# Kernel tuning notes

Hardware: AMD Instinct MI355X
Metric: run time of the kernel (lower is better)

The kernel has to match this reference:

```python
import jax, jax.numpy as jnp
import numpy as np

N_QUBITS = 10
N_LAYERS = 2
QSVT_DEGREE = 3
DT_RANK = 5  # n_qubits // 2
PI = np.float32(np.pi)

# ---- batched statevector simulation helpers (wire 0 = most significant, as in pennylane default.qubit) ----

def _apply_1q(s, wire, U):
    # s: (batch,) + (2,)*n complex; U: (batch,2,2) or (2,2)
    s = jnp.moveaxis(s, 1 + wire, 1)
    shp = s.shape
    s2 = s.reshape(shp[0], 2, -1)
    if U.ndim == 3:
        out = jnp.einsum('bij,bjr->bir', U, s2)
    else:
        out = jnp.einsum('ij,bjr->bir', U, s2)
    return jnp.moveaxis(out.reshape(shp), 1, 1 + wire)

def _ry(t):
    c = jnp.cos(t / 2).astype(jnp.complex64)
    s = jnp.sin(t / 2).astype(jnp.complex64)
    return jnp.stack([jnp.stack([c, -s], -1), jnp.stack([s, c], -1)], -2)

def _rz(t):
    e = jnp.exp(-0.5j * jnp.asarray(t).astype(jnp.complex64))
    z = jnp.zeros_like(e)
    return jnp.stack([jnp.stack([e, z], -1), jnp.stack([z, jnp.conj(e)], -1)], -2)

def _rx(t):
    c = jnp.cos(t / 2).astype(jnp.complex64)
    s = (-1j) * jnp.sin(t / 2).astype(jnp.complex64)
    return jnp.stack([jnp.stack([c, s], -1), jnp.stack([s, c], -1)], -2)

def _cnot(s, control, target):
    f = jnp.flip(s, axis=1 + target)
    s0 = jax.lax.index_in_dim(s, 0, axis=1 + control, keepdims=True)
    f1 = jax.lax.index_in_dim(f, 1, axis=1 + control, keepdims=True)
    return jnp.concatenate([s0, f1], axis=1 + control)

def _circuit(h, x, dt, cp, pc):
    """Batched selective QSVT circuit; h,x,dt: (B,n). Returns <Z_i> per wire, (B,n) float32."""
    n = N_QUBITS
    b = h.shape[0]
    s = jnp.zeros((b, 2 ** n), jnp.complex64).at[:, 0].set(1.0).reshape((b,) + (2,) * n)
    # 1. state encoding
    for i in range(n):
        s = _apply_1q(s, i, _ry(h[:, i]))
    # 2. delta-modulated QSVT block
    for d in range(QSVT_DEGREE + 1):
        for i in range(n):
            s = _apply_1q(s, i, _rz(pc[d] * dt[:, i] * PI))
        for i in range(n - 1):
            s = _cnot(s, i, i + 1)
        s = _cnot(s, n - 1, 0)
    # 3. variational block
    k = 0
    for _ in range(N_LAYERS):
        for i in range(n):
            s = _apply_1q(s, i, _rx(cp[k]))
            s = _apply_1q(s, i, _ry(cp[k + 1]))
            s = _apply_1q(s, i, _rz(cp[k + 2]))
            k += 3
        for i in range(n - 1):
            s = _cnot(s, i, i + 1)
    # 4. delta-modulated input encoding
    for i in range(n):
        s = _apply_1q(s, i, _ry(x[:, i] * dt[:, i]))
    # 5. <Z_i> measurements
    p = s.real ** 2 + s.imag ** 2
    zs = [(jax.lax.index_in_dim(p, 0, 1 + i, False) - jax.lax.index_in_dim(p, 1, 1 + i, False)).reshape(b, -1).sum(-1) for i in range(n)]
    return jnp.stack(zs, -1).astype(jnp.float32)

def setup_inputs() -> dict:
    key = jax.random.key(0)
    ks = jax.random.split(key, 6)
    B, S, n, r = 128, 512, N_QUBITS, DT_RANK
    angles = jax.random.uniform(ks[0], (B, S, n), jnp.float32) * PI  # angle encoding in [0, pi]
    W_x = jax.random.normal(ks[1], (r + 2 * n, n), jnp.float32) * 0.3  # x_proj weight (no bias)
    W_dt = jax.random.normal(ks[2], (n, r), jnp.float32) * 0.3  # dt_proj weight
    rng = np.random.default_rng(0)
    dt0 = np.exp(rng.random(n) * (np.log(0.1) - np.log(0.001)) + np.log(0.001))
    b_dt = jnp.asarray(dt0 + np.log(-np.expm1(-dt0)), jnp.float32)  # inverse-softplus init
    poly_coeffs = jax.random.normal(ks[3], (QSVT_DEGREE + 1,), jnp.float32) * 0.1
    circuit_params = jax.random.normal(ks[4], (n * N_LAYERS * 3,), jnp.float32) * 0.1
    D = jnp.ones((n,), jnp.float32)
    return {"angles": angles, "W_x": W_x, "W_dt": W_dt, "b_dt": b_dt,
            "poly_coeffs": poly_coeffs, "circuit_params": circuit_params, "D": D}

def reference(angles, W_x, W_dt, b_dt, poly_coeffs, circuit_params, D):
    # selective projections
    x_dbc = jnp.einsum('bsn,kn->bsk', angles, W_x)
    dt_raw = x_dbc[..., :DT_RANK]
    # B slice (x_dbc[..., DT_RANK:DT_RANK+n]) is computed but unused in the original forward
    C = x_dbc[..., DT_RANK + N_QUBITS:]
    dt = jax.nn.softplus(jnp.einsum('bsr,nr->bsn', dt_raw, W_dt) + b_dt)
    dt_angles = jnp.tanh(dt) * PI
    # quantum recurrence uses detached tensors in the original (torch .detach())
    x_sg = jax.lax.stop_gradient(angles)
    dt_sg = jax.lax.stop_gradient(dt_angles)
    cp = jax.lax.stop_gradient(circuit_params)
    pc = jax.lax.stop_gradient(poly_coeffs)

    def step(h, xs):
        x_t, d_t = xs
        h2 = _circuit(h, x_t, d_t, cp, pc)
        return h2, h2

    h0 = jnp.zeros((angles.shape[0], N_QUBITS), jnp.float32)
    _, hs = jax.lax.scan(step, h0, (jnp.swapaxes(x_sg, 0, 1), jnp.swapaxes(dt_sg, 0, 1)))
    hs = jnp.swapaxes(hs, 0, 1)  # (B,S,n)
    return C * hs + D * angles
```

## Files before the change

### kernel.cpp

```cpp
#include <hip/hip_runtime.h>
#include <math.h>


#define PIF 3.14159265358979323846f

constexpr int NQ = 10, SEQ = 512, NB = 128, NTHR = 256, RECF = 36;

struct CTbl { int mz[4][NQ]; };
constexpr CTbl build_tbl() {
  CTbl t{};
  unsigned mrow[NQ];
  for (int b = 0; b < NQ; ++b) mrow[b] = 1u << b;
  for (int d = 0; d < 4; ++d) {
    for (int i = 0; i < NQ; ++i) t.mz[d][i] = (int)mrow[9 - i];
    for (int i = 0; i < NQ - 1; ++i) { int bc = 9 - i, bt = 8 - i; mrow[bt] ^= mrow[bc]; }
    mrow[9] ^= mrow[0];
  }
  return t;
}
constexpr CTbl CT = build_tbl();

struct PermCols { int c4[10]; int cL[10]; };
constexpr PermCols build_perms() {
  PermCols P{};
  for (int b = 0; b < 10; ++b) {
    int x = 1 << b;
    for (int d = 0; d < 4; ++d) {
      for (int i = 0; i < 9; ++i) { int bc = 9 - i, bt = 8 - i; if ((x >> bc) & 1) x ^= (1 << bt); }
      if (x & 1) x ^= (1 << 9);
    }
    P.c4[b] = x;
    int y = 1 << b;
    for (int i = 0; i < 9; ++i) { int bc = 9 - i, bt = 8 - i; if ((y >> bc) & 1) y ^= (1 << bt); }
    P.cL[b] = y;
  }
  return P;
}
constexpr PermCols PC = build_perms();

constexpr int lanePart(int x) { return ((x >> 0) & 1) | (((x >> 5) & 1) << 1) |
                                       (((x >> 1) & 1) << 2) | (((x >> 7) & 1) << 3) |
                                       (((x >> 3) & 1) << 4) | (((x >> 9) & 1) << 5); }
constexpr int regPart2(int x)  { return ((x >> 2) & 1) | (((x >> 6) & 1) << 1); }
constexpr int wavePart(int x)  { return ((x >> 4) & 1) | (((x >> 8) & 1) << 1); }

typedef __attribute__((ext_vector_type(2))) float v2;

template<int C>
__device__ __forceinline__ int dpp1(int x) {
  return __builtin_amdgcn_update_dpp(x, x, C, 0xF, 0xF, false);
}
template<int VL>
__device__ __forceinline__ int lxi(int x) {
  if constexpr (VL == 1)  return dpp1<0xB1>(x);
  else if constexpr (VL == 2)  return dpp1<0x4E>(x);
  else if constexpr (VL == 3)  return dpp1<0x1B>(x);
  else if constexpr (VL <= 7) {
    constexpr int q = (VL & 3) ^ 3;
    int y = x;
    if constexpr (q == 1) y = dpp1<0xB1>(y);
    else if constexpr (q == 2) y = dpp1<0x4E>(y);
    else if constexpr (q == 3) y = dpp1<0x1B>(y);
    return dpp1<0x141>(y);
  } else if constexpr (VL >= 12) {
    constexpr int q = (VL & 3) ^ 3;
    int y = x;
    if constexpr (q == 1) y = dpp1<0xB1>(y);
    else if constexpr (q == 2) y = dpp1<0x4E>(y);
    else if constexpr (q == 3) y = dpp1<0x1B>(y);
    return dpp1<0x140>(y);
  } else {
    constexpr int a = VL & 3;
    int y = x;
    if constexpr (a == 1) y = dpp1<0xB1>(y);
    else if constexpr (a == 2) y = dpp1<0x4E>(y);
    else if constexpr (a == 3) y = dpp1<0x1B>(y);
    y = dpp1<0x141>(y);
    return dpp1<0x140>(y);
  }
}
template<int VL>
__device__ __forceinline__ float lx(float x) {
  if constexpr (VL == 0) return x;
  else if constexpr (VL & 32) {
    int addr = (((int)threadIdx.x & 63) ^ VL) << 2;
    return __int_as_float(__builtin_amdgcn_ds_bpermute(addr, __float_as_int(x)));
  } else if constexpr (VL & 16) {
    return __int_as_float(__builtin_amdgcn_ds_swizzle(__float_as_int(x), (VL << 10) | 0x1F));
  } else {
    return __int_as_float(lxi<VL>(__float_as_int(x)));
  }
}
__device__ __forceinline__ float rdl(float x, int l) {
  return __int_as_float(__builtin_amdgcn_readlane(__float_as_int(x), l));
}

__device__ __forceinline__ void apply4(v2* amp, const v2* p, bool par, float4 U0, float4 U1) {
  v2 u00 = {U0.x, U0.y}, u01 = {U0.z, U0.w}, u10 = {U1.x, U1.y}, u11 = {U1.z, U1.w};
  v2 A = par ? u11 : u00, B = par ? u10 : u01;
  v2 An = {-A.y, A.y}, Bn = {-B.y, B.y};
#pragma unroll
  for (int r = 0; r < 4; ++r) {
    v2 o = amp[r], q = p[r];
    v2 res = A.x * o;
    res += An * __builtin_shufflevector(o, o, 1, 0);
    res += B.x * q;
    res += Bn * __builtin_shufflevector(q, q, 1, 0);
    amp[r] = res;
  }
}

template<int VL>
__device__ __forceinline__ void gate_lane(v2* amp, float4 U0, float4 U1, int lane) {
  v2 p[4];
#pragma unroll
  for (int r = 0; r < 4; ++r) { p[r].x = lx<VL>(amp[r].x); p[r].y = lx<VL>(amp[r].y); }
  apply4(amp, p, (lane & VL) != 0, U0, U1);
}

template<int VR>
__device__ __forceinline__ void gate_reg(v2* amp, float4 U0, float4 U1) {
  v2 p[4];
#pragma unroll
  for (int r = 0; r < 4; ++r) p[r] = amp[r ^ VR];
  v2 u00 = {U0.x, U0.y}, u01 = {U0.z, U0.w}, u10 = {U1.x, U1.y}, u11 = {U1.z, U1.w};
#pragma unroll
  for (int r = 0; r < 4; ++r) {
    const bool par = (r & VR) != 0;
    v2 A = par ? u11 : u00, B = par ? u10 : u01;
    v2 An = {-A.y, A.y}, Bn = {-B.y, B.y};
    v2 o = amp[r], q = p[r];
    v2 res = A.x * o;
    res += An * __builtin_shufflevector(o, o, 1, 0);
    res += B.x * q;
    res += Bn * __builtin_shufflevector(q, q, 1, 0);
    amp[r] = res;
  }
}

__device__ __forceinline__ void gate_wave(v2* amp, float4 U0, float4 U1,
                                          v2* exb, int wbase, int pbase, bool par) {
#pragma unroll
  for (int r = 0; r < 4; ++r) exb[r * 256 + wbase] = amp[r];
  __syncthreads();
  v2 p[4];
#pragma unroll
  for (int r = 0; r < 4; ++r) p[r] = exb[r * 256 + pbase];
  apply4(amp, p, par, U0, U1);
}

__device__ __forceinline__ void permute(v2* amp, v2* buf, int dbase, int o1, int o2, int oidx) {
  buf[dbase]           = amp[0];
  buf[dbase ^ o1]      = amp[1];
  buf[dbase ^ o2]      = amp[2];
  buf[dbase ^ o1 ^ o2] = amp[3];
  __syncthreads();
  amp[0] = buf[oidx];
  amp[1] = buf[oidx | 4];
  amp[2] = buf[oidx | 64];
  amp[3] = buf[oidx | 68];
}

template<int VL>
__device__ __forceinline__ float xdot_lane(const v2* amp) {
  v2 acc = {0.f, 0.f};
#pragma unroll
  for (int r = 0; r < 4; ++r) {
    v2 p; p.x = lx<VL>(amp[r].x); p.y = lx<VL>(amp[r].y);
    acc += amp[r] * p;
  }
  return acc.x + acc.y;
}
template<int VR>
__device__ __forceinline__ float xdot_reg(const v2* amp) {
  v2 acc = {0.f, 0.f};
#pragma unroll
  for (int r = 0; r < 4; ++r) acc += amp[r] * amp[r ^ VR];
  return acc.x + acc.y;
}

__global__ __launch_bounds__(NTHR, 1) void qmamba_main(
    const float* __restrict__ angles, const float* __restrict__ Wx,
    const float* __restrict__ Wdt, const float* __restrict__ bdt,
    const float* __restrict__ pc, const float* __restrict__ cp,
    float* __restrict__ out)
{
  __shared__ float  tblL[SEQ][RECF];
  __shared__ float4 uuL[40];
  __shared__ v2     ex0[1024];
  __shared__ v2     ex1[1024];
  __shared__ float  zb[4][16];

  const int tid  = threadIdx.x;
  const int lane = tid & 63;
  const int wave = tid >> 6;
  const int b    = blockIdx.x;

  if (tid < 20) {
    int k = tid * 3;
    float al = 0.5f * cp[k], be = 0.5f * cp[k + 1], ga = 0.5f * cp[k + 2];
    float ca = __cosf(al), sa = __sinf(al);
    float cb = __cosf(be), sb = __sinf(be);
    float cg = __cosf(ga), sg = __sinf(ga);
    float2 M00 = make_float2(cb * ca,  sb * sa);
    float2 M01 = make_float2(-sb * ca, -cb * sa);
    float2 M10 = make_float2(sb * ca,  -cb * sa);
    float2 M11 = make_float2(cb * ca,  -sb * sa);
    float2 e0 = make_float2(cg, -sg), e1 = make_float2(cg, sg);
    auto cm = [](float2 a, float2 c) {
      return make_float2(a.x * c.x - a.y * c.y, a.x * c.y + a.y * c.x);
    };
    float2 u00 = cm(M00, e0), u01 = cm(M01, e0), u10 = cm(M10, e1), u11 = cm(M11, e1);
    uuL[2 * tid]     = make_float4(u00.x, u00.y, u01.x, u01.y);
    uuL[2 * tid + 1] = make_float4(u10.x, u10.y, u11.x, u11.y);
  }

#pragma unroll 1
  for (int k = 0; k < 2; ++k) {
    const int t = k * NTHR + tid;
    const float* ar = angles + (size_t)(b * SEQ + t) * NQ;
    float a[NQ];
#pragma unroll
    for (int n = 0; n < NQ; ++n) a[n] = ar[n];
    float dtr[5];
#pragma unroll
    for (int r = 0; r < 5; ++r) {
      float acc = 0.f;
#pragma unroll
      for (int n = 0; n < NQ; ++n) acc += a[n] * Wx[r * NQ + n];
      dtr[r] = acc;
    }
    float* rec = &tblL[t][0];
#pragma unroll
    for (int w = 0; w < NQ; ++w) {
      float lin = bdt[w];
#pragma unroll
      for (int r = 0; r < 5; ++r) lin += dtr[r] * Wdt[w * 5 + r];
      float sp = lin > 0.f ? lin + log1pf(__expf(-lin)) : log1pf(__expf(lin));
      float th = tanhf(sp) * PIF;
      float fa = a[w] * th;
      rec[w]      = th;
      rec[12 + w] = __cosf(fa);
      rec[24 + w] = __sinf(fa);
    }
  }
  __syncthreads();

  float pch[4];
#pragma unroll
  for (int d = 0; d < 4; ++d) pch[d] = 0.5f * pc[d] * PIF;

  unsigned PW0 = 0, PW1 = 0;
#pragma unroll
  for (int k = 0; k < 40; ++k) {
    const int m  = CT.mz[k / 10][k % 10];
    const int lm = lanePart(m), wm = wavePart(m);
    unsigned flip = ((unsigned)((__popc(lane & lm) ^ __popc(wave & wm)) & 1)) ^ 1u;
    if (k < 32) PW0 |= flip << k; else PW1 |= flip << (k - 32);
  }

  int d4 = 0, dL = 0;
  if (lane & 1)  { d4 ^= PC.c4[0]; dL ^= PC.cL[0]; }
  if (lane & 2)  { d4 ^= PC.c4[5]; dL ^= PC.cL[5]; }
  if (lane & 4)  { d4 ^= PC.c4[1]; dL ^= PC.cL[1]; }
  if (lane & 8)  { d4 ^= PC.c4[7]; dL ^= PC.cL[7]; }
  if (lane & 16) { d4 ^= PC.c4[3]; dL ^= PC.cL[3]; }
  if (lane & 32) { d4 ^= PC.c4[9]; dL ^= PC.cL[9]; }
  if (wave & 1)  { d4 ^= PC.c4[4]; dL ^= PC.cL[4]; }
  if (wave & 2)  { d4 ^= PC.c4[8]; dL ^= PC.cL[8]; }

  const int oidx = (lane & 1) | (((lane >> 1) & 1) << 5) | (((lane >> 2) & 1) << 1)
                 | (((lane >> 3) & 1) << 7) | (((lane >> 4) & 1) << 3) | (((lane >> 5) & 1) << 9)
                 | ((wave & 1) << 4) | (((wave >> 1) & 1) << 8);

  const int wbase = wave * 64 + lane;
  const int pb1   = (wave ^ 1) * 64 + lane;
  const int pb2   = (wave ^ 2) * 64 + lane;

  float hcw[NQ], hsw[NQ];
#pragma unroll
  for (int w = 0; w < NQ; ++w) { hcw[w] = 1.f; hsw[w] = 0.f; }

  v2 amp[4];

#pragma unroll 1
  for (int t = 0; t < SEQ; ++t) {
    float tha[12];
    {
      const float4* rq = (const float4*)&tblL[t][0];
#pragma unroll
      for (int j = 0; j < 3; ++j) ((float4*)tha)[j] = rq[j];
    }

    float F;
    F  = (lane & 1)  ? hsw[9] : hcw[9];
    F *= (lane & 2)  ? hsw[4] : hcw[4];
    F *= (lane & 4)  ? hsw[8] : hcw[8];
    F *= (lane & 8)  ? hsw[2] : hcw[2];
    F *= (lane & 16) ? hsw[6] : hcw[6];
    F *= (lane & 32) ? hsw[0] : hcw[0];
    F *= (wave & 1)  ? hsw[5] : hcw[5];
    F *= (wave & 2)  ? hsw[1] : hcw[1];
    const float G0 = F * hcw[7] * hcw[3];
    const float G1 = F * hsw[7] * hcw[3];
    const float G2 = F * hcw[7] * hsw[3];
    const float G3 = F * hsw[7] * hsw[3];

    float S[4] = {0.f, 0.f, 0.f, 0.f};
#pragma unroll
    for (int k = 0; k < 40; ++k) {
      const int m  = CT.mz[k / 10][k % 10];
      const int gr = regPart2(m);
      float v = pch[k / 10] * tha[k % 10];
      unsigned fl = ((k < 32 ? (PW0 >> k) : (PW1 >> (k - 32))) & 1u) << 31;
      S[gr] += __int_as_float(__float_as_int(v) ^ fl);
    }
    {
      float a0 = S[0], a1 = S[1], a2 = S[2], a3 = S[3];
      float b0 = a0 + a1, b1 = a0 - a1, b2 = a2 + a3, b3 = a2 - a3;
      S[0] = b0 + b2; S[2] = b0 - b2; S[1] = b1 + b3; S[3] = b1 - b3;
    }
    {
      float sn, cs;
      __sincosf(S[0], &sn, &cs); amp[0].x = G0 * cs; amp[0].y = G0 * sn;
      __sincosf(S[1], &sn, &cs); amp[1].x = G1 * cs; amp[1].y = G1 * sn;
      __sincosf(S[2], &sn, &cs); amp[2].x = G2 * cs; amp[2].y = G2 * sn;
      __sincosf(S[3], &sn, &cs); amp[3].x = G3 * cs; amp[3].y = G3 * sn;
    }

    permute(amp, ex0, d4, PC.c4[2], PC.c4[6], oidx);

    gate_lane<32>(amp, uuL[0],  uuL[1],  lane);
    gate_wave    (amp, uuL[2],  uuL[3],  ex1, wbase, pb2, (wave & 2) != 0);
    gate_lane<8> (amp, uuL[4],  uuL[5],  lane);
    gate_reg<2>  (amp, uuL[6],  uuL[7]);
    gate_lane<2> (amp, uuL[8],  uuL[9],  lane);
    gate_wave    (amp, uuL[10], uuL[11], ex0, wbase, pb1, (wave & 1) != 0);
    gate_lane<16>(amp, uuL[12], uuL[13], lane);
    gate_reg<1>  (amp, uuL[14], uuL[15]);
    gate_lane<4> (amp, uuL[16], uuL[17], lane);
    gate_lane<1> (amp, uuL[18], uuL[19], lane);

    permute(amp, ex1, dL, PC.cL[2], PC.cL[6], oidx);

    gate_lane<32>(amp, uuL[20], uuL[21], lane);
    gate_wave    (amp, uuL[22], uuL[23], ex0, wbase, pb2, (wave & 2) != 0);
    gate_lane<8> (amp, uuL[24], uuL[25], lane);
    gate_reg<2>  (amp, uuL[26], uuL[27]);
    gate_lane<2> (amp, uuL[28], uuL[29], lane);
    gate_wave    (amp, uuL[30], uuL[31], ex1, wbase, pb1, (wave & 1) != 0);
    gate_lane<16>(amp, uuL[32], uuL[33], lane);
    gate_reg<1>  (amp, uuL[34], uuL[35]);
    gate_lane<4> (amp, uuL[36], uuL[37], lane);
    gate_lane<1> (amp, uuL[38], uuL[39], lane);

    permute(amp, ex0, dL, PC.cL[2], PC.cL[6], oidx);

    float cfv[12], sfv[12];
    {
      const float4* rq = (const float4*)&tblL[t][0];
#pragma unroll
      for (int j = 0; j < 3; ++j) { ((float4*)cfv)[j] = rq[3 + j]; ((float4*)sfv)[j] = rq[6 + j]; }
    }

    float T[4];
#pragma unroll
    for (int r = 0; r < 4; ++r) T[r] = amp[r].x * amp[r].x + amp[r].y * amp[r].y;
    {
      float a0 = T[0], a1 = T[1], a2 = T[2], a3 = T[3];
      float b0 = a0 + a1, b1 = a0 - a1, b2 = a2 + a3, b3 = a2 - a3;
      T[0] = b0 + b2; T[2] = b0 - b2; T[1] = b1 + b3; T[3] = b1 - b3;
    }

    v2 pw1[4], pw5[4];
    {
#pragma unroll
      for (int r = 0; r < 4; ++r) ex1[r * 256 + wbase] = amp[r];
      __syncthreads();
#pragma unroll
      for (int r = 0; r < 4; ++r) pw1[r] = ex1[r * 256 + pb2];
#pragma unroll
      for (int r = 0; r < 4; ++r) pw5[r] = ex1[r * 256 + pb1];
    }

    float zv[NQ];
    { float zp = (lane & 32) ? -T[0] : T[0]; zv[0] = cfv[0] * zp - sfv[0] * xdot_lane<32>(amp); }
    { float zp = (wave & 2)  ? -T[0] : T[0];
      v2 acc = {0.f, 0.f};
#pragma unroll
      for (int r = 0; r < 4; ++r) acc += amp[r] * pw1[r];
      zv[1] = cfv[1] * zp - sfv[1] * (acc.x + acc.y); }
    { float zp = (lane & 8)  ? -T[0] : T[0]; zv[2] = cfv[2] * zp - sfv[2] * xdot_lane<8>(amp); }
    { zv[3] = cfv[3] * T[2] - sfv[3] * xdot_reg<2>(amp); }
    { float zp = (lane & 2)  ? -T[0] : T[0]; zv[4] = cfv[4] * zp - sfv[4] * xdot_lane<2>(amp); }
    { float zp = (wave & 1)  ? -T[0] : T[0];
      v2 acc = {0.f, 0.f};
#pragma unroll
      for (int r = 0; r < 4; ++r) acc += amp[r] * pw5[r];
      zv[5] = cfv[5] * zp - sfv[5] * (acc.x + acc.y); }
    { float zp = (lane & 16) ? -T[0] : T[0]; zv[6] = cfv[6] * zp - sfv[6] * xdot_lane<16>(amp); }
    { zv[7] = cfv[7] * T[1] - sfv[7] * xdot_reg<1>(amp); }
    { float zp = (lane & 4)  ? -T[0] : T[0]; zv[8] = cfv[8] * zp - sfv[8] * xdot_lane<4>(amp); }
    { float zp = (lane & 1)  ? -T[0] : T[0]; zv[9] = cfv[9] * zp - sfv[9] * xdot_lane<1>(amp); }

#pragma unroll
    for (int w = 0; w < NQ; ++w) {
      zv[w] += lx<1>(zv[w]);
      zv[w] += lx<2>(zv[w]);
      zv[w] += lx<4>(zv[w]);
    }
    const int l7 = lane & 7;
    float c01 = (l7 & 1) ? zv[1] : zv[0];
    float c23 = (l7 & 1) ? zv[3] : zv[2];
    float c45 = (l7 & 1) ? zv[5] : zv[4];
    float c67 = (l7 & 1) ? zv[7] : zv[6];
    float c03 = (l7 & 2) ? c23 : c01;
    float c47 = (l7 & 2) ? c67 : c45;
    float pk  = (l7 & 4) ? c47 : c03;
    pk += lx<8>(pk);  pk += lx<16>(pk);  pk += lx<32>(pk);
    float z8 = zv[8]; z8 += lx<8>(z8); z8 += lx<16>(z8); z8 += lx<32>(z8);
    float z9 = zv[9]; z9 += lx<8>(z9); z9 += lx<16>(z9); z9 += lx<32>(z9);
    float zsel = pk;
    zsel = (lane == 8) ? z8 : zsel;
    zsel = (lane == 9) ? z9 : zsel;

    if (lane < NQ) zb[wave][lane] = zsel;
    __syncthreads();
    float z = 0.f;
    if (lane < NQ) {
      z = zb[0][lane] + zb[1][lane] + zb[2][lane] + zb[3][lane];
      if (wave == 0) out[(size_t)(b * SEQ + t) * NQ + lane] = z;
    }
    float sn_h, cs_h;
    __sincosf(0.5f * z, &sn_h, &cs_h);
#pragma unroll
    for (int w = 0; w < NQ; ++w) { hcw[w] = rdl(cs_h, w); hsw[w] = rdl(sn_h, w); }
  }
}

__global__ __launch_bounds__(256) void qmamba_post(
    const float* __restrict__ angles, const float* __restrict__ Wx,
    const float* __restrict__ Dg, float* __restrict__ out)
{
  int i = blockIdx.x * 256 + threadIdx.x;
  if (i >= NB * SEQ * NQ) return;
  int w  = i % NQ;
  int bt = i / NQ;
  const float* a = angles + (size_t)bt * NQ;
  float C = 0.f;
#pragma unroll
  for (int n = 0; n < NQ; ++n) C += a[n] * Wx[(15 + w) * NQ + n];
  float z = out[i];
  out[i] = C * z + Dg[w] * a[w];
}

extern "C" void kernel_launch(void* const* d_in, const int* in_sizes, int n_in,
                              void* d_out, int out_size, void* d_ws, size_t ws_size,
                              hipStream_t stream) {
  (void)in_sizes; (void)n_in; (void)out_size; (void)d_ws; (void)ws_size;
  const float* angles = (const float*)d_in[0];
  const float* Wx     = (const float*)d_in[1];
  const float* Wdt    = (const float*)d_in[2];
  const float* bdt    = (const float*)d_in[3];
  const float* pc     = (const float*)d_in[4];
  const float* cp     = (const float*)d_in[5];
  const float* Dg     = (const float*)d_in[6];
  float* out = (float*)d_out;
  hipLaunchKernelGGL(qmamba_main, dim3(NB), dim3(NTHR), 0, stream,
                     angles, Wx, Wdt, bdt, pc, cp, out);
  hipLaunchKernelGGL(qmamba_post, dim3((NB * SEQ * NQ + 255) / 256), dim3(256), 0, stream,
                     angles, Wx, Dg, out);
}
```

Baseline: 2.477 ms.

## Spread statevector over 8 waves and fuse cross-wave gates into permutation gathers

Doubles the block to 512 threads so each thread holds 2 amplitudes instead of 4, moving one more qubit into the wave index. The three cross-wave single-qubit gates per layer are folded into precomputed 8-term combination coefficients that are applied while gathering after the CNOT permutation through shared memory. This removes the separate gate_wave shared-memory round trips and barriers, and the LDS indexing is XOR-swizzled to avoid bank conflicts. In exchange each thread does 16 LDS reads per permutation, and the larger block adds synchronisation cost across 8 waves, with per-wave partial sums reduced over 8 slots.

```diff
diff --git a/kernel.cpp b/kernel.cpp
--- a/kernel.cpp
+++ b/kernel.cpp
@@ -4,7 +4,7 @@
 
 #define PIF 3.14159265358979323846f
 
-constexpr int NQ = 10, SEQ = 512, NB = 128, NTHR = 256, RECF = 36;
+constexpr int NQ = 10, SEQ = 512, NB = 128, NTHR = 512, RECF = 36;
 
 struct CTbl { int mz[4][NQ]; };
 constexpr CTbl build_tbl() {
@@ -38,13 +38,15 @@
 }
 constexpr PermCols PC = build_perms();
 
-constexpr int lanePart(int x) { return ((x >> 0) & 1) | (((x >> 5) & 1) << 1) |
-                                       (((x >> 1) & 1) << 2) | (((x >> 7) & 1) << 3) |
-                                       (((x >> 3) & 1) << 4) | (((x >> 9) & 1) << 5); }
-constexpr int regPart2(int x)  { return ((x >> 2) & 1) | (((x >> 6) & 1) << 1); }
-constexpr int wavePart(int x)  { return ((x >> 4) & 1) | (((x >> 8) & 1) << 1); }
+constexpr int lanePart(int x)  { return ((x >> 0) & 1) | (((x >> 5) & 1) << 1) |
+                                        (((x >> 1) & 1) << 2) | (((x >> 7) & 1) << 3) |
+                                        (((x >> 3) & 1) << 4) | (((x >> 9) & 1) << 5); }
+constexpr int wavePart8(int x) { return ((x >> 4) & 1) | (((x >> 8) & 1) << 1) |
+                                        (((x >> 6) & 1) << 2); }
 
 typedef __attribute__((ext_vector_type(2))) float v2;
+
+constexpr int VOFS[8] = {0, 16, 256, 272, 64, 80, 320, 336};
 
 template<int C>
 __device__ __forceinline__ int dpp1(int x) {
@@ -95,12 +97,16 @@
   return __int_as_float(__builtin_amdgcn_readlane(__float_as_int(x), l));
 }
 
-__device__ __forceinline__ void apply4(v2* amp, const v2* p, bool par, float4 U0, float4 U1) {
+__device__ __forceinline__ int swz(int j) {
+  return j ^ (((j >> 5) & 1) << 2) ^ ((j >> 7) & 1);
+}
+
+__device__ __forceinline__ void apply2(v2* amp, const v2* p, bool par, float4 U0, float4 U1) {
   v2 u00 = {U0.x, U0.y}, u01 = {U0.z, U0.w}, u10 = {U1.x, U1.y}, u11 = {U1.z, U1.w};
   v2 A = par ? u11 : u00, B = par ? u10 : u01;
   v2 An = {-A.y, A.y}, Bn = {-B.y, B.y};
 #pragma unroll
-  for (int r = 0; r < 4; ++r) {
+  for (int r = 0; r < 2; ++r) {
     v2 o = amp[r], q = p[r];
     v2 res = A.x * o;
     res += An * __builtin_shufflevector(o, o, 1, 0);
@@ -111,75 +117,36 @@
 }
 
 template<int VL>
-__device__ __forceinline__ void gate_lane(v2* amp, float4 U0, float4 U1, int lane) {
-  v2 p[4];
-#pragma unroll
-  for (int r = 0; r < 4; ++r) { p[r].x = lx<VL>(amp[r].x); p[r].y = lx<VL>(amp[r].y); }
-  apply4(amp, p, (lane & VL) != 0, U0, U1);
-}
-
-template<int VR>
-__device__ __forceinline__ void gate_reg(v2* amp, float4 U0, float4 U1) {
-  v2 p[4];
-#pragma unroll
-  for (int r = 0; r < 4; ++r) p[r] = amp[r ^ VR];
+__device__ __forceinline__ void gate_lane2(v2* amp, float4 U0, float4 U1, int lane) {
+  v2 p[2];
+#pragma unroll
+  for (int r = 0; r < 2; ++r) { p[r].x = lx<VL>(amp[r].x); p[r].y = lx<VL>(amp[r].y); }
+  apply2(amp, p, (lane & VL) != 0, U0, U1);
+}
+
+__device__ __forceinline__ void gate_reg1(v2* amp, float4 U0, float4 U1) {
   v2 u00 = {U0.x, U0.y}, u01 = {U0.z, U0.w}, u10 = {U1.x, U1.y}, u11 = {U1.z, U1.w};
-#pragma unroll
-  for (int r = 0; r < 4; ++r) {
-    const bool par = (r & VR) != 0;
-    v2 A = par ? u11 : u00, B = par ? u10 : u01;
-    v2 An = {-A.y, A.y}, Bn = {-B.y, B.y};
-    v2 o = amp[r], q = p[r];
-    v2 res = A.x * o;
-    res += An * __builtin_shufflevector(o, o, 1, 0);
-    res += B.x * q;
-    res += Bn * __builtin_shufflevector(q, q, 1, 0);
-    amp[r] = res;
-  }
-}
-
-__device__ __forceinline__ void gate_wave(v2* amp, float4 U0, float4 U1,
-                                          v2* exb, int wbase, int pbase, bool par) {
-#pragma unroll
-  for (int r = 0; r < 4; ++r) exb[r * 256 + wbase] = amp[r];
-  __syncthreads();
-  v2 p[4];
-#pragma unroll
-  for (int r = 0; r < 4; ++r) p[r] = exb[r * 256 + pbase];
-  apply4(amp, p, par, U0, U1);
-}
-
-__device__ __forceinline__ void permute(v2* amp, v2* buf, int dbase, int o1, int o2, int oidx) {
-  buf[dbase]           = amp[0];
-  buf[dbase ^ o1]      = amp[1];
-  buf[dbase ^ o2]      = amp[2];
-  buf[dbase ^ o1 ^ o2] = amp[3];
-  __syncthreads();
-  amp[0] = buf[oidx];
-  amp[1] = buf[oidx | 4];
-  amp[2] = buf[oidx | 64];
-  amp[3] = buf[oidx | 68];
+  v2 o0 = amp[0], o1 = amp[1];
+  v2 a0 = {0.f, 0.f}, a1 = {0.f, 0.f};
+  a0.x += u00.x * o0.x - u00.y * o0.y;  a0.y += u00.x * o0.y + u00.y * o0.x;
+  a0.x += u01.x * o1.x - u01.y * o1.y;  a0.y += u01.x * o1.y + u01.y * o1.x;
+  a1.x += u10.x * o0.x - u10.y * o0.y;  a1.y += u10.x * o0.y + u10.y * o0.x;
+  a1.x += u11.x * o1.x - u11.y * o1.y;  a1.y += u11.x * o1.y + u11.y * o1.x;
+  amp[0] = a0; amp[1] = a1;
 }
 
 template<int VL>
-__device__ __forceinline__ float xdot_lane(const v2* amp) {
+__device__ __forceinline__ float xdot_lane2(const v2* amp) {
   v2 acc = {0.f, 0.f};
 #pragma unroll
-  for (int r = 0; r < 4; ++r) {
+  for (int r = 0; r < 2; ++r) {
     v2 p; p.x = lx<VL>(amp[r].x); p.y = lx<VL>(amp[r].y);
     acc += amp[r] * p;
   }
   return acc.x + acc.y;
 }
-template<int VR>
-__device__ __forceinline__ float xdot_reg(const v2* amp) {
-  v2 acc = {0.f, 0.f};
-#pragma unroll
-  for (int r = 0; r < 4; ++r) acc += amp[r] * amp[r ^ VR];
-  return acc.x + acc.y;
-}
-
-__global__ __launch_bounds__(NTHR, 1) void qmamba_main(
+
+__global__ __launch_bounds__(NTHR, 2) void qmamba_main(
     const float* __restrict__ angles, const float* __restrict__ Wx,
     const float* __restrict__ Wdt, const float* __restrict__ bdt,
     const float* __restrict__ pc, const float* __restrict__ cp,
@@ -189,7 +156,7 @@
   __shared__ float4 uuL[40];
   __shared__ v2     ex0[1024];
   __shared__ v2     ex1[1024];
-  __shared__ float  zb[4][16];
+  __shared__ float  zb[8][16];
 
   const int tid  = threadIdx.x;
   const int lane = tid & 63;
@@ -215,9 +182,8 @@
     uuL[2 * tid + 1] = make_float4(u10.x, u10.y, u11.x, u11.y);
   }
 
-#pragma unroll 1
-  for (int k = 0; k < 2; ++k) {
-    const int t = k * NTHR + tid;
+  {
+    const int t = tid;
     const float* ar = angles + (size_t)(b * SEQ + t) * NQ;
     float a[NQ];
 #pragma unroll
@@ -250,11 +216,29 @@
 #pragma unroll
   for (int d = 0; d < 4; ++d) pch[d] = 0.5f * pc[d] * PIF;
 
+  v2 cw0[8], cw1[8];
+  {
+    const int s5 = wave & 1, s1 = (wave >> 1) & 1, s3 = (wave >> 2) & 1;
+    auto ent = [&](int g, int row, int col) -> v2 {
+      float4 R = uuL[2 * g + row];
+      return col ? v2{R.z, R.w} : v2{R.x, R.y};
+    };
+    auto cmul = [](v2 a, v2 c) -> v2 {
+      return v2{a.x * c.x - a.y * c.y, a.x * c.y + a.y * c.x};
+    };
+#pragma unroll
+    for (int v = 0; v < 8; ++v) {
+      const int v5 = v & 1, v1 = (v >> 1) & 1, v3 = (v >> 2) & 1;
+      cw0[v] = cmul(cmul(ent(5,  s5, s5 ^ v5), ent(1,  s1, s1 ^ v1)), ent(3,  s3, s3 ^ v3));
+      cw1[v] = cmul(cmul(ent(15, s5, s5 ^ v5), ent(11, s1, s1 ^ v1)), ent(13, s3, s3 ^ v3));
+    }
+  }
+
   unsigned PW0 = 0, PW1 = 0;
 #pragma unroll
   for (int k = 0; k < 40; ++k) {
     const int m  = CT.mz[k / 10][k % 10];
-    const int lm = lanePart(m), wm = wavePart(m);
+    const int lm = lanePart(m), wm = wavePart8(m);
     unsigned flip = ((unsigned)((__popc(lane & lm) ^ __popc(wave & wm)) & 1)) ^ 1u;
     if (k < 32) PW0 |= flip << k; else PW1 |= flip << (k - 32);
   }
@@ -268,20 +252,18 @@
   if (lane & 32) { d4 ^= PC.c4[9]; dL ^= PC.cL[9]; }
   if (wave & 1)  { d4 ^= PC.c4[4]; dL ^= PC.cL[4]; }
   if (wave & 2)  { d4 ^= PC.c4[8]; dL ^= PC.cL[8]; }
+  if (wave & 4)  { d4 ^= PC.c4[6]; dL ^= PC.cL[6]; }
+  const int oR4 = PC.c4[2], oRL = PC.cL[2];
 
   const int oidx = (lane & 1) | (((lane >> 1) & 1) << 5) | (((lane >> 2) & 1) << 1)
                  | (((lane >> 3) & 1) << 7) | (((lane >> 4) & 1) << 3) | (((lane >> 5) & 1) << 9)
-                 | ((wave & 1) << 4) | (((wave >> 1) & 1) << 8);
-
-  const int wbase = wave * 64 + lane;
-  const int pb1   = (wave ^ 1) * 64 + lane;
-  const int pb2   = (wave ^ 2) * 64 + lane;
+                 | ((wave & 1) << 4) | (((wave >> 1) & 1) << 8) | (((wave >> 2) & 1) << 6);
 
   float hcw[NQ], hsw[NQ];
 #pragma unroll
   for (int w = 0; w < NQ; ++w) { hcw[w] = 1.f; hsw[w] = 0.f; }
 
-  v2 amp[4];
+  v2 amp[2];
 
 #pragma unroll 1
   for (int t = 0; t < SEQ; ++t) {
@@ -301,60 +283,94 @@
     F *= (lane & 32) ? hsw[0] : hcw[0];
     F *= (wave & 1)  ? hsw[5] : hcw[5];
     F *= (wave & 2)  ? hsw[1] : hcw[1];
-    const float G0 = F * hcw[7] * hcw[3];
-    const float G1 = F * hsw[7] * hcw[3];
-    const float G2 = F * hcw[7] * hsw[3];
-    const float G3 = F * hsw[7] * hsw[3];
-
-    float S[4] = {0.f, 0.f, 0.f, 0.f};
+    F *= (wave & 4)  ? hsw[3] : hcw[3];
+    const float G0 = F * hcw[7];
+    const float G1 = F * hsw[7];
+
+    float S0 = 0.f, S1 = 0.f;
 #pragma unroll
     for (int k = 0; k < 40; ++k) {
       const int m  = CT.mz[k / 10][k % 10];
-      const int gr = regPart2(m);
       float v = pch[k / 10] * tha[k % 10];
       unsigned fl = ((k < 32 ? (PW0 >> k) : (PW1 >> (k - 32))) & 1u) << 31;
-      S[gr] += __int_as_float(__float_as_int(v) ^ fl);
-    }
-    {
-      float a0 = S[0], a1 = S[1], a2 = S[2], a3 = S[3];
-      float b0 = a0 + a1, b1 = a0 - a1, b2 = a2 + a3, b3 = a2 - a3;
-      S[0] = b0 + b2; S[2] = b0 - b2; S[1] = b1 + b3; S[3] = b1 - b3;
+      float sv = __int_as_float(__float_as_int(v) ^ fl);
+      if ((m >> 2) & 1) S1 += sv; else S0 += sv;
     }
     {
       float sn, cs;
-      __sincosf(S[0], &sn, &cs); amp[0].x = G0 * cs; amp[0].y = G0 * sn;
-      __sincosf(S[1], &sn, &cs); amp[1].x = G1 * cs; amp[1].y = G1 * sn;
-      __sincosf(S[2], &sn, &cs); amp[2].x = G2 * cs; amp[2].y = G2 * sn;
-      __sincosf(S[3], &sn, &cs); amp[3].x = G3 * cs; amp[3].y = G3 * sn;
-    }
-
-    permute(amp, ex0, d4, PC.c4[2], PC.c4[6], oidx);
-
-    gate_lane<32>(amp, uuL[0],  uuL[1],  lane);
-    gate_wave    (amp, uuL[2],  uuL[3],  ex1, wbase, pb2, (wave & 2) != 0);
-    gate_lane<8> (amp, uuL[4],  uuL[5],  lane);
-    gate_reg<2>  (amp, uuL[6],  uuL[7]);
-    gate_lane<2> (amp, uuL[8],  uuL[9],  lane);
-    gate_wave    (amp, uuL[10], uuL[11], ex0, wbase, pb1, (wave & 1) != 0);
-    gate_lane<16>(amp, uuL[12], uuL[13], lane);
-    gate_reg<1>  (amp, uuL[14], uuL[15]);
-    gate_lane<4> (amp, uuL[16], uuL[17], lane);
-    gate_lane<1> (amp, uuL[18], uuL[19], lane);
-
-    permute(amp, ex1, dL, PC.cL[2], PC.cL[6], oidx);
-
-    gate_lane<32>(amp, uuL[20], uuL[21], lane);
-    gate_wave    (amp, uuL[22], uuL[23], ex0, wbase, pb2, (wave & 2) != 0);
-    gate_lane<8> (amp, uuL[24], uuL[25], lane);
-    gate_reg<2>  (amp, uuL[26], uuL[27]);
-    gate_lane<2> (amp, uuL[28], uuL[29], lane);
-    gate_wave    (amp, uuL[30], uuL[31], ex1, wbase, pb1, (wave & 1) != 0);
-    gate_lane<16>(amp, uuL[32], uuL[33], lane);
-    gate_reg<1>  (amp, uuL[34], uuL[35]);
-    gate_lane<4> (amp, uuL[36], uuL[37], lane);
-    gate_lane<1> (amp, uuL[38], uuL[39], lane);
-
-    permute(amp, ex0, dL, PC.cL[2], PC.cL[6], oidx);
+      __sincosf(S0 + S1, &sn, &cs); amp[0].x = G0 * cs; amp[0].y = G0 * sn;
+      __sincosf(S0 - S1, &sn, &cs); amp[1].x = G1 * cs; amp[1].y = G1 * sn;
+    }
+
+    ex0[swz(d4)]       = amp[0];
+    ex0[swz(d4 ^ oR4)] = amp[1];
+    __syncthreads();
+    {
+      v2 pv0[8], pv1[8];
+#pragma unroll
+      for (int v = 0; v < 8; ++v) {
+        const int base = oidx ^ VOFS[v];
+        pv0[v] = ex0[swz(base)];
+        pv1[v] = ex0[swz(base | 4)];
+      }
+      v2 a0 = {0.f, 0.f}, a1 = {0.f, 0.f};
+#pragma unroll
+      for (int v = 0; v < 8; ++v) {
+        v2 c = cw0[v];
+        a0.x += c.x * pv0[v].x - c.y * pv0[v].y;
+        a0.y += c.x * pv0[v].y + c.y * pv0[v].x;
+        a1.x += c.x * pv1[v].x - c.y * pv1[v].y;
+        a1.y += c.x * pv1[v].y + c.y * pv1[v].x;
+      }
+      amp[0] = a0; amp[1] = a1;
+    }
+    gate_lane2<32>(amp, uuL[0],  uuL[1],  lane);
+    gate_lane2<8> (amp, uuL[4],  uuL[5],  lane);
+    gate_lane2<2> (amp, uuL[8],  uuL[9],  lane);
+    gate_lane2<16>(amp, uuL[12], uuL[13], lane);
+    gate_reg1     (amp, uuL[14], uuL[15]);
+    gate_lane2<4> (amp, uuL[16], uuL[17], lane);
+    gate_lane2<1> (amp, uuL[18], uuL[19], lane);
+
+    ex1[swz(dL)]       = amp[0];
+    ex1[swz(dL ^ oRL)] = amp[1];
+    __syncthreads();
+    {
+      v2 pv0[8], pv1[8];
+#pragma unroll
+      for (int v = 0; v < 8; ++v) {
+        const int base = oidx ^ VOFS[v];
+        pv0[v] = ex1[swz(base)];
+        pv1[v] = ex1[swz(base | 4)];
+      }
+      v2 a0 = {0.f, 0.f}, a1 = {0.f, 0.f};
+#pragma unroll
+      for (int v = 0; v < 8; ++v) {
+        v2 c = cw1[v];
+        a0.x += c.x * pv0[v].x - c.y * pv0[v].y;
+        a0.y += c.x * pv0[v].y + c.y * pv0[v].x;
+        a1.x += c.x * pv1[v].x - c.y * pv1[v].y;
+        a1.y += c.x * pv1[v].y + c.y * pv1[v].x;
+      }
+      amp[0] = a0; amp[1] = a1;
+    }
+    gate_lane2<32>(amp, uuL[20], uuL[21], lane);
+    gate_lane2<8> (amp, uuL[24], uuL[25], lane);
+    gate_lane2<2> (amp, uuL[28], uuL[29], lane);
+    gate_lane2<16>(amp, uuL[32], uuL[33], lane);
+    gate_reg1     (amp, uuL[34], uuL[35]);
+    gate_lane2<4> (amp, uuL[36], uuL[37], lane);
+    gate_lane2<1> (amp, uuL[38], uuL[39], lane);
+
+    ex0[swz(dL)]       = amp[0];
+    ex0[swz(dL ^ oRL)] = amp[1];
+    __syncthreads();
+    v2 pw5[2], pw1[2], pw3[2];
+    amp[0] = ex0[swz(oidx)];
+    amp[1] = ex0[swz(oidx | 4)];
+    pw5[0] = ex0[swz(oidx ^ 16)];   pw5[1] = ex0[swz((oidx ^ 16) | 4)];
+    pw1[0] = ex0[swz(oidx ^ 256)];  pw1[1] = ex0[swz((oidx ^ 256) | 4)];
+    pw3[0] = ex0[swz(oidx ^ 64)];   pw3[1] = ex0[swz((oidx ^ 64) | 4)];
 
     float cfv[12], sfv[12];
     {
@@ -363,45 +379,28 @@
       for (int j = 0; j < 3; ++j) { ((float4*)cfv)[j] = rq[3 + j]; ((float4*)sfv)[j] = rq[6 + j]; }
     }
 
-    float T[4];
-#pragma unroll
-    for (int r = 0; r < 4; ++r) T[r] = amp[r].x * amp[r].x + amp[r].y * amp[r].y;
-    {
-      float a0 = T[0], a1 = T[1], a2 = T[2], a3 = T[3];
-      float b0 = a0 + a1, b1 = a0 - a1, b2 = a2 + a3, b3 = a2 - a3;
-      T[0] = b0 + b2; T[2] = b0 - b2; T[1] = b1 + b3; T[3] = b1 - b3;
-    }
-
-    v2 pw1[4], pw5[4];
-    {
-#pragma unroll
-      for (int r = 0; r < 4; ++r) ex1[r * 256 + wbase] = amp[r];
-      __syncthreads();
-#pragma unroll
-      for (int r = 0; r < 4; ++r) pw1[r] = ex1[r * 256 + pb2];
-#pragma unroll
-      for (int r = 0; r < 4; ++r) pw5[r] = ex1[r * 256 + pb1];
-    }
+    const float n0 = amp[0].x * amp[0].x + amp[0].y * amp[0].y;
+    const float n1 = amp[1].x * amp[1].x + amp[1].y * amp[1].y;
+    const float T0 = n0 + n1;
+    const float T1 = n0 - n1;
+
+    auto vdot2 = [](const v2* a, const v2* p) {
+      v2 acc = a[0] * p[0] + a[1] * p[1];
+      return acc.x + acc.y;
+    };
 
     float zv[NQ];
-    { float zp = (lane & 32) ? -T[0] : T[0]; zv[0] = cfv[0] * zp - sfv[0] * xdot_lane<32>(amp); }
-    { float zp = (wave & 2)  ? -T[0] : T[0];
-      v2 acc = {0.f, 0.f};
-#pragma unroll
-      for (int r = 0; r < 4; ++r) acc += amp[r] * pw1[r];
-      zv[1] = cfv[1] * zp - sfv[1] * (acc.x + acc.y); }
-    { float zp = (lane & 8)  ? -T[0] : T[0]; zv[2] = cfv[2] * zp - sfv[2] * xdot_lane<8>(amp); }
-    { zv[3] = cfv[3] * T[2] - sfv[3] * xdot_reg<2>(amp); }
-    { float zp = (lane & 2)  ? -T[0] : T[0]; zv[4] = cfv[4] * zp - sfv[4] * xdot_lane<2>(amp); }
-    { float zp = (wave & 1)  ? -T[0] : T[0];
-      v2 acc = {0.f, 0.f};
-#pragma unroll
-      for (int r = 0; r < 4; ++r) acc += amp[r] * pw5[r];
-      zv[5] = cfv[5] * zp - sfv[5] * (acc.x + acc.y); }
-    { float zp = (lane & 16) ? -T[0] : T[0]; zv[6] = cfv[6] * zp - sfv[6] * xdot_lane<16>(amp); }
-    { zv[7] = cfv[7] * T[1] - sfv[7] * xdot_reg<1>(amp); }
-    { float zp = (lane & 4)  ? -T[0] : T[0]; zv[8] = cfv[8] * zp - sfv[8] * xdot_lane<4>(amp); }
-    { float zp = (lane & 1)  ? -T[0] : T[0]; zv[9] = cfv[9] * zp - sfv[9] * xdot_lane<1>(amp); }
+    { float zp = (lane & 32) ? -T0 : T0; zv[0] = cfv[0] * zp - sfv[0] * xdot_lane2<32>(amp); }
+    { float zp = (wave & 2)  ? -T0 : T0; zv[1] = cfv[1] * zp - sfv[1] * vdot2(amp, pw1); }
+    { float zp = (lane & 8)  ? -T0 : T0; zv[2] = cfv[2] * zp - sfv[2] * xdot_lane2<8>(amp); }
+    { float zp = (wave & 4)  ? -T0 : T0; zv[3] = cfv[3] * zp - sfv[3] * vdot2(amp, pw3); }
+    { float zp = (lane & 2)  ? -T0 : T0; zv[4] = cfv[4] * zp - sfv[4] * xdot_lane2<2>(amp); }
+    { float zp = (wave & 1)  ? -T0 : T0; zv[5] = cfv[5] * zp - sfv[5] * vdot2(amp, pw5); }
+    { float zp = (lane & 16) ? -T0 : T0; zv[6] = cfv[6] * zp - sfv[6] * xdot_lane2<16>(amp); }
+    { float xr = 2.f * (amp[0].x * amp[1].x + amp[0].y * amp[1].y);
+      zv[7] = cfv[7] * T1 - sfv[7] * xr; }
+    { float zp = (lane & 4)  ? -T0 : T0; zv[8] = cfv[8] * zp - sfv[8] * xdot_lane2<4>(amp); }
+    { float zp = (lane & 1)  ? -T0 : T0; zv[9] = cfv[9] * zp - sfv[9] * xdot_lane2<1>(amp); }
 
 #pragma unroll
     for (int w = 0; w < NQ; ++w) {
@@ -428,7 +427,8 @@
     __syncthreads();
     float z = 0.f;
     if (lane < NQ) {
-      z = zb[0][lane] + zb[1][lane] + zb[2][lane] + zb[3][lane];
+      z = zb[0][lane] + zb[1][lane] + zb[2][lane] + zb[3][lane]
+        + zb[4][lane] + zb[5][lane] + zb[6][lane] + zb[7][lane];
       if (wave == 0) out[(size_t)(b * SEQ + t) * NQ + lane] = z;
     }
     float sn_h, cs_h;
```

New measurement: 2.221 ms. 1.12x faster.
